# Performance work log

Measured on AMD Instinct MI355X. Metric: run time of the kernel, lower is better.

## Reference

```python
import jax, jax.numpy as jnp
import numpy as np

N = 20000   # nodes
D = 64      # emb_dim
H = 512     # 8 * emb_dim
E = 320000  # edges per graph


def setup_inputs() -> dict:
    key = jax.random.key(0)
    ks = jax.random.split(key, 40)
    i = iter(range(40))
    def nrm(shape, s=0.05):
        return jax.random.normal(ks[next(i)], shape, dtype=jnp.float32) * s
    def edges():
        return jax.random.randint(ks[next(i)], (E,), 0, N, dtype=jnp.int32)
    inp = {}
    inp['k_emb'] = nrm((N, D), 1.0)
    inp['pr_src'] = edges(); inp['pr_dst'] = edges()
    inp['pr_ew'] = jax.random.uniform(ks[next(i)], (E,), dtype=jnp.float32)
    inp['cc_src'] = edges(); inp['cc_dst'] = edges()
    inp['cc_ew'] = jax.random.uniform(ks[next(i)], (E,), dtype=jnp.float32)
    inp['sps_src'] = edges(); inp['sps_dst'] = edges()
    inp['pr_Ws0'] = nrm((D, H)); inp['pr_Wn0'] = nrm((D, H)); inp['pr_b0'] = jnp.zeros((H,), jnp.float32)
    inp['pr_Ws1'] = nrm((H, D)); inp['pr_Wn1'] = nrm((H, D)); inp['pr_b1'] = jnp.zeros((D,), jnp.float32)
    inp['cc_Ws0'] = nrm((D, H)); inp['cc_Wn0'] = nrm((D, H)); inp['cc_b0'] = jnp.zeros((H,), jnp.float32)
    inp['cc_Ws1'] = nrm((H, D)); inp['cc_Wn1'] = nrm((H, D)); inp['cc_b1'] = jnp.zeros((D,), jnp.float32)
    inp['ap_Ws0'] = nrm((D, D)); inp['ap_Wn0'] = nrm((D, D)); inp['ap_b0'] = jnp.zeros((D,), jnp.float32)
    inp['ap_Ws1'] = nrm((D, D)); inp['ap_Wn1'] = nrm((D, D)); inp['ap_b1'] = jnp.zeros((D,), jnp.float32)
    inp['att_W'] = nrm((D, D)); inp['att_b'] = jnp.zeros((D,), jnp.float32)
    return inp


def _sage(x, src, dst, ew, Ws, Wn, b):
    # DGL SAGEConv 'mean': neigh = sum(w_e * h_src) / in_degree; out = x@Ws + neigh@Wn + b
    msg = x[src]                                  # [E, din] gather
    if ew is not None:
        msg = msg * ew[:, None]
    agg = jax.ops.segment_sum(msg, dst, num_segments=N)            # [N, din]
    deg = jax.ops.segment_sum(jnp.ones((msg.shape[0],), x.dtype), dst, num_segments=N)
    agg = agg / jnp.maximum(deg, 1.0)[:, None]
    return x @ Ws + agg @ Wn + b


def reference(k_emb, pr_src, pr_dst, pr_ew, cc_src, cc_dst, cc_ew, sps_src, sps_dst,
              pr_Ws0, pr_Wn0, pr_b0, pr_Ws1, pr_Wn1, pr_b1,
              cc_Ws0, cc_Wn0, cc_b0, cc_Ws1, cc_Wn1, cc_b1,
              ap_Ws0, ap_Wn0, ap_b0, ap_Ws1, ap_Wn1, ap_b1,
              att_W, att_b):
    pr = jax.nn.relu(_sage(k_emb, pr_src, pr_dst, pr_ew, pr_Ws0, pr_Wn0, pr_b0))
    pr = _sage(pr, pr_src, pr_dst, pr_ew, pr_Ws1, pr_Wn1, pr_b1)            # [N, D]
    cc = jax.nn.relu(_sage(k_emb, cc_src, cc_dst, cc_ew, cc_Ws0, cc_Wn0, cc_b0))
    cc = _sage(cc, cc_src, cc_dst, cc_ew, cc_Ws1, cc_Wn1, cc_b1)            # [N, D]
    ap = jax.nn.relu(_sage(k_emb, sps_src, sps_dst, None, ap_Ws0, ap_Wn0, ap_b0))
    ap = _sage(ap, sps_src, sps_dst, None, ap_Ws1, ap_Wn1, ap_b1)           # [N, D]
    # APATT fusion
    z = jnp.stack((pr, cc), axis=1)                      # [N, 2, D]
    proj = jnp.tanh(z @ att_W + att_b)                   # [N, 2, D]
    w = jnp.sum(ap[:, None, :] * proj, axis=-1, keepdims=True).mean(0)  # [2, 1]
    beta = jax.nn.softmax(w, axis=0)                     # [2, 1]
    return (beta * z).sum(axis=1)                        # [N, D]
```

## Files before the change

kernel.cpp:

```cpp
#include <hip/hip_runtime.h>

#define NN 20000
#define NP 20032
#define DD 64
#define HH 512
#define EE 320000
#define ATT_BLOCKS 625
#define BLOCKS_E (EE / 256)
#define CB 157
#define EPB 4096
#define B1_BLOCKS ((EE + EPB - 1) / EPB)
#define ZERO_N (3 * NN + 3 * CB)
#define ZERO_BLOCKS ((ZERO_N + 255) / 256)

typedef __attribute__((ext_vector_type(8))) short short8;
typedef __attribute__((ext_vector_type(4))) float f32x4;

__device__ __forceinline__ ushort f2bf(float f) {
    union { float f; unsigned u; } v; v.f = f;
    unsigned r = v.u + 0x7FFF + ((v.u >> 16) & 1);
    return (ushort)(r >> 16);
}
__device__ __forceinline__ float bf2f(ushort h) {
    union { unsigned u; float f; } v; v.u = ((unsigned)h) << 16;
    return v.f;
}

__global__ __launch_bounds__(256) void hist3(const int* __restrict__ d0,
                                             const int* __restrict__ d1,
                                             const int* __restrict__ d2,
                                             int* __restrict__ cnt) {
    int g = blockIdx.x / BLOCKS_E;
    int e = (blockIdx.x % BLOCKS_E) * 256 + threadIdx.x;
    const int* d = (g == 0) ? d0 : (g == 1) ? d1 : d2;
    if (e < EE) atomicAdd(&cnt[g * NN + d[e]], 1);
}

__global__ __launch_bounds__(1024) void scan_kernel(const int* __restrict__ cnt,
                                                    int* __restrict__ rowptr,
                                                    float* __restrict__ invd) {
    __shared__ int part[1024];
    int g = blockIdx.x;
    const int* c = cnt + g * NN;
    int* rp = rowptr + g * (NN + 1);
    int tid = threadIdx.x;
    const int CH = (NN + 1023) / 1024;
    int i0 = tid * CH;
    int s = 0;
    for (int i = 0; i < CH; ++i) { int idx = i0 + i; if (idx < NN) s += c[idx]; }
    part[tid] = s;
    __syncthreads();
    for (int off = 1; off < 1024; off <<= 1) {
        int v = (tid >= off) ? part[tid - off] : 0;
        __syncthreads();
        part[tid] += v;
        __syncthreads();
    }
    int run = (tid > 0) ? part[tid - 1] : 0;
    for (int i = 0; i < CH; ++i) {
        int idx = i0 + i;
        if (idx < NN) {
            int cv = c[idx];
            rp[idx] = run; run += cv;
            invd[g * NN + idx] = 1.0f / fmaxf((float)cv, 1.0f);
        }
    }
    if (tid == 1023) rp[NN] = part[1023];
}

__global__ __launch_bounds__(256) void bucket_coarse(
    const int* __restrict__ s0, const int* __restrict__ d0, const float* __restrict__ w0,
    const int* __restrict__ s1, const int* __restrict__ d1, const float* __restrict__ w1,
    const int* __restrict__ s2, const int* __restrict__ d2,
    const int* __restrict__ rowptr,
    int* __restrict__ ccur,
    int2* __restrict__ ce,
    ushort* __restrict__ cd) {
    __shared__ int cnt_s[CB];
    __shared__ int off_s[CB];
    __shared__ int pos_s[CB];
    __shared__ int gbase[CB];
    __shared__ int lsrc[EPB];
    __shared__ int lew[EPB];
    __shared__ ushort ldst[EPB];
    int g = blockIdx.x / B1_BLOCKS;
    int blk = blockIdx.x % B1_BLOCKS;
    const int* S = (g == 0) ? s0 : (g == 1) ? s1 : s2;
    const int* D = (g == 0) ? d0 : (g == 1) ? d1 : d2;
    const float* W = (g == 0) ? w0 : (g == 1) ? w1 : nullptr;
    int e0 = blk * EPB;
    int n = min(EPB, EE - e0);
    for (int i = threadIdx.x; i < CB; i += 256) cnt_s[i] = 0;
    __syncthreads();
    for (int i = threadIdx.x; i < n; i += 256)
        atomicAdd(&cnt_s[D[e0 + i] >> 7], 1);
    __syncthreads();
    if (threadIdx.x == 0) {
        int run = 0;
        for (int i = 0; i < CB; ++i) { off_s[i] = run; run += cnt_s[i]; }
    }
    __syncthreads();
    if (threadIdx.x < CB) pos_s[threadIdx.x] = off_s[threadIdx.x];
    __syncthreads();
    for (int i = threadIdx.x; i < n; i += 256) {
        int e = e0 + i;
        int d = D[e];
        int p = atomicAdd(&pos_s[d >> 7], 1);
        lsrc[p] = S[e];
        lew[p] = (g < 2) ? __float_as_int(W[e]) : 0;
        ldst[p] = (ushort)d;
    }
    __syncthreads();
    if (threadIdx.x < CB)
        gbase[threadIdx.x] = atomicAdd(&ccur[g * CB + threadIdx.x], cnt_s[threadIdx.x]);
    __syncthreads();
    const int* rp = rowptr + g * (NN + 1);
    for (int j = threadIdx.x; j < n; j += 256) {
        ushort d = ldst[j];
        int cb = d >> 7;
        int gpos = rp[cb << 7] + gbase[cb] + (j - off_s[cb]);
        ce[(size_t)g * EE + gpos] = make_int2(lsrc[j], lew[j]);
        cd[(size_t)g * EE + gpos] = d;
    }
}

__global__ __launch_bounds__(256) void bucket_fine(
    const int* __restrict__ rowptr,
    const int2* __restrict__ ce, const ushort* __restrict__ cd,
    int2* __restrict__ edge_s,
    int* __restrict__ src_s2) {
    __shared__ int rp_s[129];
    __shared__ int cur_s[128];
    int g = blockIdx.x / CB;
    int cb = blockIdx.x % CB;
    const int* rp = rowptr + g * (NN + 1);
    int n0 = cb << 7;
    int n1 = min(n0 + 128, NN);
    int m = n1 - n0;
    if (threadIdx.x <= m) rp_s[threadIdx.x] = rp[n0 + threadIdx.x];
    if (threadIdx.x < m) cur_s[threadIdx.x] = 0;
    __syncthreads();
    int beg = rp_s[0], end = rp_s[m];
    for (int j = beg + threadIdx.x; j < end; j += 256) {
        int2 e = ce[(size_t)g * EE + j];
        int dl = (int)cd[(size_t)g * EE + j] - n0;
        int pos = rp_s[dl] + atomicAdd(&cur_s[dl], 1);
        if (g < 2) edge_s[(size_t)g * EE + pos] = e;
        else src_s2[pos] = e.x;
    }
}

__global__ __launch_bounds__(256) void pull_cast3(const ushort* __restrict__ xh,
                                                  const int* __restrict__ rowptr,
                                                  const int2* __restrict__ edge_s,
                                                  const int* __restrict__ src_s2,
                                                  const float* __restrict__ invd,
                                                  ushort* __restrict__ aggh) {
    int wid = (blockIdx.x * blockDim.x + threadIdx.x) >> 6;
    int lane = threadIdx.x & 63;
    if (wid >= 3 * NN) return;
    int g = wid / NN, n = wid % NN;
    const int* rp = rowptr + g * (NN + 1);
    int beg = rp[n], end = rp[n + 1];
    float a[8] = {};
    int i = beg;
    if (g < 2) {
        const int2* es = edge_s + (size_t)g * EE;
        for (; i + 8 <= end; i += 8) {
#pragma unroll
            for (int j = 0; j < 8; ++j) {
                int2 e = es[i + j];
                a[j] = fmaf(bf2f(xh[e.x * DD + lane]), __int_as_float(e.y), a[j]);
            }
        }
        for (; i < end; ++i) {
            int2 e = es[i];
            a[0] = fmaf(bf2f(xh[e.x * DD + lane]), __int_as_float(e.y), a[0]);
        }
    } else {
        for (; i + 8 <= end; i += 8) {
#pragma unroll
            for (int j = 0; j < 8; ++j)
                a[j] += bf2f(xh[src_s2[i + j] * DD + lane]);
        }
        for (; i < end; ++i) a[0] += bf2f(xh[src_s2[i] * DD + lane]);
    }
    float acc = ((a[0] + a[1]) + (a[2] + a[3])) + ((a[4] + a[5]) + (a[6] + a[7]));
    aggh[((size_t)g * NP + n) * 64 + lane] = f2bf(acc * invd[g * NN + n]);
}

__global__ __launch_bounds__(256) void pull_combine3(const ushort* __restrict__ xnh,
                                                     const int* __restrict__ rowptr,
                                                     const int2* __restrict__ edge_s,
                                                     const int* __restrict__ src_s2,
                                                     const float* __restrict__ invd,
                                                     const float* __restrict__ b_pr,
                                                     const float* __restrict__ b_cc,
                                                     const float* __restrict__ b_ap,
                                                     float* __restrict__ o_pr,
                                                     float* __restrict__ o_cc,
                                                     float* __restrict__ o_ap) {
    int wid = (blockIdx.x * blockDim.x + threadIdx.x) >> 6;
    int lane = threadIdx.x & 63;
    if (wid >= 3 * NN) return;
    int g = wid / NN, n = wid % NN;
    const int* rp = rowptr + g * (NN + 1);
    const ushort* x = xnh + (size_t)g * NP * 64;
    const float* bias = (g == 0) ? b_pr : (g == 1) ? b_cc : b_ap;
    float* out = (g == 0) ? o_pr : (g == 1) ? o_cc : o_ap;
    int beg = rp[n], end = rp[n + 1];
    float a[8] = {};
    int i = beg;
    if (g < 2) {
        const int2* es = edge_s + (size_t)g * EE;
        for (; i + 8 <= end; i += 8) {
#pragma unroll
            for (int j = 0; j < 8; ++j) {
                int2 e = es[i + j];
                a[j] = fmaf(bf2f(x[e.x * DD + lane]), __int_as_float(e.y), a[j]);
            }
        }
        for (; i < end; ++i) {
            int2 e = es[i];
            a[0] = fmaf(bf2f(x[e.x * DD + lane]), __int_as_float(e.y), a[0]);
        }
    } else {
        for (; i + 8 <= end; i += 8) {
#pragma unroll
            for (int j = 0; j < 8; ++j)
                a[j] += bf2f(x[src_s2[i + j] * DD + lane]);
        }
        for (; i < end; ++i) a[0] += bf2f(x[src_s2[i] * DD + lane]);
    }
    float acc = ((a[0] + a[1]) + (a[2] + a[3])) + ((a[4] + a[5]) + (a[6] + a[7]));
    out[n * DD + lane] += acc * invd[g * NN + n] + bias[lane];
}

__global__ __launch_bounds__(256) void pack_all(
    const float* __restrict__ pr_Ws0, const float* __restrict__ pr_Wn0,
    const float* __restrict__ cc_Ws0, const float* __restrict__ cc_Wn0,
    const float* __restrict__ pr_Ws1, const float* __restrict__ pr_Wn1,
    const float* __restrict__ cc_Ws1, const float* __restrict__ cc_Wn1,
    const float* __restrict__ ap_Ws0, const float* __restrict__ ap_Wn0,
    const float* __restrict__ ap_Ws1, const float* __restrict__ ap_Wn1,
    const float* __restrict__ k_emb,
    ushort* __restrict__ W0h_pr, ushort* __restrict__ W0h_cc,
    ushort* __restrict__ W1h_pr, ushort* __restrict__ W1h_cc,
    ushort* __restrict__ W0h_ap, ushort* __restrict__ W1h_ap,
    ushort* __restrict__ xh,
    int* __restrict__ zero_base) {
    int b = blockIdx.x;
    int tid = threadIdx.x;
    if (b < 512) {
        int t = (b & 255) * 256 + tid;
        const float* Ws = (b < 256) ? pr_Ws0 : cc_Ws0;
        const float* Wn = (b < 256) ? pr_Wn0 : cc_Wn0;
        ushort* o = (b < 256) ? W0h_pr : W0h_cc;
        int c = t >> 7, k = t & 127;
        o[t] = f2bf((k < 64) ? Ws[k * 512 + c] : Wn[(k - 64) * 512 + c]);
    } else if (b < 1024) {
        int t = ((b - 512) & 255) * 256 + tid;
        const float* Ws = (b < 768) ? pr_Ws1 : cc_Ws1;
        const float* Wn = (b < 768) ? pr_Wn1 : cc_Wn1;
        ushort* o = (b < 768) ? W1h_pr : W1h_cc;
        int c = t >> 9, k = t & 511;
        o[t] = f2bf((c < 64) ? Ws[k * 64 + c] : Wn[k * 64 + (c - 64)]);
    } else if (b < 1056) {
        int t = (b - 1024) * 256 + tid;
        int c = t >> 7, k = t & 127;
        W0h_ap[t] = f2bf((k < 64) ? ap_Ws0[k * 64 + c] : ap_Wn0[(k - 64) * 64 + c]);
    } else if (b < 1088) {
        int t = (b - 1056) * 256 + tid;
        int c = t >> 6, k = t & 63;
        W1h_ap[t] = f2bf((c < 64) ? ap_Ws1[k * 64 + c] : ap_Wn1[k * 64 + (c - 64)]);
    } else if (b < 1088 + ZERO_BLOCKS) {
        int t = (b - 1088) * 256 + tid;
        if (t < ZERO_N) zero_base[t] = 0;
    } else {
        int t = (b - 1088 - ZERO_BLOCKS) * 256 + tid;
        if (t < NN * DD) xh[t] = f2bf(k_emb[t]);
    }
}

__global__ __launch_bounds__(512, 4) void fused_sage4(
    const ushort* __restrict__ xh,
    const ushort* __restrict__ aggA,
    const ushort* __restrict__ W0a, const ushort* __restrict__ W1a,
    const ushort* __restrict__ W0b, const ushort* __restrict__ W1b,
    const float* __restrict__ b0a, const float* __restrict__ b0b,
    float* __restrict__ outS0, float* __restrict__ outS1,
    ushort* __restrict__ xnh, int nblk) {
    constexpr int LROW = 136;
    __shared__ ushort Ahs[64 * LROW];
    __shared__ ushort h1s[64 * LROW];
    int br = blockIdx.x / nblk;
    int rb = blockIdx.x % nblk;
    const ushort* W0 = br ? W0b : W0a;
    const ushort* W1 = br ? W1b : W1a;
    const float* b0 = br ? b0b : b0a;
    float* outS = br ? outS1 : outS0;
    ushort* outX = xnh + (size_t)br * NP * 64;
    const ushort* agg = aggA + (size_t)br * NP * 64;
    int row0 = rb * 64;

    int wv = threadIdx.x >> 6;
    int lane = threadIdx.x & 63;
    int lrow = lane & 15;
    int koff = (lane >> 4) * 8;
    int crow = (lane >> 4) * 4;

    {
        int r = threadIdx.x >> 3;
        int seg = threadIdx.x & 7;
        const ushort* src = (seg < 4) ? (xh + (size_t)(row0 + r) * 64 + seg * 16)
                                      : (agg + (size_t)(row0 + r) * 64 + (seg - 4) * 16);
        *(short8*)&Ahs[r * LROW + seg * 16] = *(const short8*)src;
        *(short8*)&Ahs[r * LROW + seg * 16 + 8] = *(const short8*)(src + 8);
    }
    __syncthreads();

    f32x4 C[4] = {};
#pragma unroll
    for (int p = 0; p < 4; ++p) {
        {
            short8 B[4];
#pragma unroll
            for (int kk = 0; kk < 4; ++kk)
                B[kk] = *(const short8*)(W0 + (size_t)(p * 128 + wv * 16 + lrow) * 128 + kk * 32 + koff);
            f32x4 acc[4] = {};
#pragma unroll
            for (int rg = 0; rg < 4; ++rg) {
#pragma unroll
                for (int kk = 0; kk < 4; ++kk) {
                    short8 a = *(const short8*)&Ahs[(rg * 16 + lrow) * LROW + kk * 32 + koff];
                    acc[rg] = __builtin_amdgcn_mfma_f32_16x16x32_bf16(a, B[kk], acc[rg], 0, 0, 0);
                }
            }
            float bb = b0[p * 128 + wv * 16 + lrow];
#pragma unroll
            for (int rg = 0; rg < 4; ++rg) {
#pragma unroll
                for (int r = 0; r < 4; ++r) {
                    float v = fmaxf(acc[rg][r] + bb, 0.0f);
                    h1s[(rg * 16 + crow + r) * LROW + wv * 16 + lrow] = f2bf(v);
                }
            }
        }
        __syncthreads();
        {
            short8 B[4];
#pragma unroll
            for (int kc = 0; kc < 4; ++kc)
                B[kc] = *(const short8*)(W1 + (size_t)(wv * 16 + lrow) * HH + p * 128 + kc * 32 + koff);
#pragma unroll
            for (int rg = 0; rg < 4; ++rg) {
#pragma unroll
                for (int kc = 0; kc < 4; ++kc) {
                    short8 a = *(const short8*)&h1s[(rg * 16 + lrow) * LROW + kc * 32 + koff];
                    C[rg] = __builtin_amdgcn_mfma_f32_16x16x32_bf16(a, B[kc], C[rg], 0, 0, 0);
                }
            }
        }
        __syncthreads();
    }
    int col = wv * 16 + lrow;
    if (col < 64) {
        float* o = outS + col;
#pragma unroll
        for (int rg = 0; rg < 4; ++rg)
#pragma unroll
            for (int r = 0; r < 4; ++r) {
                int row = row0 + rg * 16 + crow + r;
                if (row < NN) o[(size_t)row * 64] = C[rg][r];
            }
    } else {
        ushort* o = outX + (col - 64);
#pragma unroll
        for (int rg = 0; rg < 4; ++rg)
#pragma unroll
            for (int r = 0; r < 4; ++r) {
                int row = row0 + rg * 16 + crow + r;
                if (row < NN) o[(size_t)row * 64] = f2bf(C[rg][r]);
            }
    }
}

__global__ __launch_bounds__(256, 4) void fused_sage_ap(
    const ushort* __restrict__ xh,
    const ushort* __restrict__ agg,
    const ushort* __restrict__ W0,
    const ushort* __restrict__ W1,
    const float* __restrict__ b0,
    float* __restrict__ outS,
    ushort* __restrict__ outX) {
    constexpr int LROW = 72;
    __shared__ ushort h1s[16 * LROW];
    int wv = threadIdx.x >> 6;
    int lane = threadIdx.x & 63;
    int lrow = lane & 15;
    int koff = (lane >> 4) * 8;
    int crow = (lane >> 4) * 4;
    int row0 = blockIdx.x * 16;

    {
        const size_t aoff = (size_t)(row0 + lrow) * 64 + koff;
        short8 aF[4];
#pragma unroll
        for (int kk = 0; kk < 2; ++kk) {
            aF[kk]     = *(const short8*)(xh + aoff + kk * 32);
            aF[2 + kk] = *(const short8*)(agg + aoff + kk * 32);
        }
        f32x4 acc = {};
#pragma unroll
        for (int kk = 0; kk < 4; ++kk) {
            short8 b = *(const short8*)(W0 + (size_t)(wv * 16 + lrow) * 128 + kk * 32 + koff);
            acc = __builtin_amdgcn_mfma_f32_16x16x32_bf16(aF[kk], b, acc, 0, 0, 0);
        }
        float bb = b0[wv * 16 + lrow];
#pragma unroll
        for (int r = 0; r < 4; ++r) {
            h1s[(crow + r) * LROW + wv * 16 + lrow] = f2bf(fmaxf(acc[r] + bb, 0.0f));
        }
    }
    __syncthreads();
    {
        f32x4 C2[2] = {};
#pragma unroll
        for (int kc = 0; kc < 2; ++kc) {
            short8 a = *(const short8*)&h1s[lrow * LROW + kc * 32 + koff];
#pragma unroll
            for (int c = 0; c < 2; ++c) {
                short8 b = *(const short8*)(W1 + (size_t)(wv * 32 + c * 16 + lrow) * 64 + kc * 32 + koff);
                C2[c] = __builtin_amdgcn_mfma_f32_16x16x32_bf16(a, b, C2[c], 0, 0, 0);
            }
        }
#pragma unroll
        for (int c = 0; c < 2; ++c) {
            int col = wv * 32 + c * 16 + lrow;
#pragma unroll
            for (int r = 0; r < 4; ++r) {
                int row = row0 + crow + r;
                if (row < NN) {
                    if (col < 64) outS[(size_t)row * 64 + col] = C2[c][r];
                    else outX[(size_t)row * 64 + (col - 64)] = f2bf(C2[c][r]);
                }
            }
        }
    }
}

__global__ __launch_bounds__(256) void att_stage1(const float* __restrict__ pr,
                                                  const float* __restrict__ cc,
                                                  const float* __restrict__ ap,
                                                  const float* __restrict__ attW,
                                                  const float* __restrict__ attb,
                                                  float2* __restrict__ partial) {
    __shared__ float red[8];
    int lane = threadIdx.x & 63;
    int wv = threadIdx.x >> 6;
    int gw = blockIdx.x * 4 + wv;
    const int nwaves = ATT_BLOCKS * 4;
    float b = attb[lane];
    float c0 = 0.f, c1 = 0.f;
    for (int n = gw; n < NN; n += nwaves) {
        float p0 = 0.f, p1 = 0.f;
        for (int k = 0; k < DD; ++k) {
            float w = attW[k * DD + lane];
            p0 = fmaf(pr[n * DD + k], w, p0);
            p1 = fmaf(cc[n * DD + k], w, p1);
        }
        float a = ap[n * DD + lane];
        c0 += a * tanhf(p0 + b);
        c1 += a * tanhf(p1 + b);
    }
#pragma unroll
    for (int off = 32; off; off >>= 1) {
        c0 += __shfl_xor(c0, off);
        c1 += __shfl_xor(c1, off);
    }
    if (lane == 0) { red[wv * 2] = c0; red[wv * 2 + 1] = c1; }
    __syncthreads();
    if (threadIdx.x == 0) {
        partial[blockIdx.x] = make_float2(red[0] + red[2] + red[4] + red[6],
                                          red[1] + red[3] + red[5] + red[7]);
    }
}

__global__ __launch_bounds__(64) void att_stage2(const float2* __restrict__ partial,
                                                 float* __restrict__ w_acc) {
    int lane = threadIdx.x;
    float s0 = 0.f, s1 = 0.f;
    for (int i = lane; i < ATT_BLOCKS; i += 64) {
        float2 p = partial[i];
        s0 += p.x; s1 += p.y;
    }
#pragma unroll
    for (int off = 32; off; off >>= 1) {
        s0 += __shfl_xor(s0, off);
        s1 += __shfl_xor(s1, off);
    }
    if (lane == 0) { w_acc[0] = s0; w_acc[1] = s1; }
}

__global__ __launch_bounds__(256) void final_kernel(float* __restrict__ pr_out,
                                                    const float* __restrict__ cc,
                                                    const float* __restrict__ w_acc) {
    int t = blockIdx.x * blockDim.x + threadIdx.x;
    if (t >= NN * DD) return;
    float w0 = w_acc[0] * (1.0f / NN);
    float w1 = w_acc[1] * (1.0f / NN);
    float m = fmaxf(w0, w1);
    float e0 = __expf(w0 - m), e1 = __expf(w1 - m);
    float inv = 1.0f / (e0 + e1);
    pr_out[t] = (e0 * pr_out[t] + e1 * cc[t]) * inv;
}

extern "C" void kernel_launch(void* const* d_in, const int* in_sizes, int n_in,
                              void* d_out, int out_size, void* d_ws, size_t ws_size,
                              hipStream_t stream) {
    const float* k_emb  = (const float*)d_in[0];
    const int*   pr_src = (const int*)d_in[1];
    const int*   pr_dst = (const int*)d_in[2];
    const float* pr_ew  = (const float*)d_in[3];
    const int*   cc_src = (const int*)d_in[4];
    const int*   cc_dst = (const int*)d_in[5];
    const float* cc_ew  = (const float*)d_in[6];
    const int*   sps_src = (const int*)d_in[7];
    const int*   sps_dst = (const int*)d_in[8];
    const float* pr_Ws0 = (const float*)d_in[9];
    const float* pr_Wn0 = (const float*)d_in[10];
    const float* pr_b0  = (const float*)d_in[11];
    const float* pr_Ws1 = (const float*)d_in[12];
    const float* pr_Wn1 = (const float*)d_in[13];
    const float* pr_b1  = (const float*)d_in[14];
    const float* cc_Ws0 = (const float*)d_in[15];
    const float* cc_Wn0 = (const float*)d_in[16];
    const float* cc_b0  = (const float*)d_in[17];
    const float* cc_Ws1 = (const float*)d_in[18];
    const float* cc_Wn1 = (const float*)d_in[19];
    const float* cc_b1  = (const float*)d_in[20];
    const float* ap_Ws0 = (const float*)d_in[21];
    const float* ap_Wn0 = (const float*)d_in[22];
    const float* ap_b0  = (const float*)d_in[23];
    const float* ap_Ws1 = (const float*)d_in[24];
    const float* ap_Wn1 = (const float*)d_in[25];
    const float* ap_b1  = (const float*)d_in[26];
    const float* att_W  = (const float*)d_in[27];
    const float* att_b  = (const float*)d_in[28];
    float* out = (float*)d_out;

    char* base = (char*)d_ws;
    size_t off = 0;
    auto alloc = [&](size_t bytes) -> void* {
        void* p = base + off;
        off = (off + bytes + 255) & ~(size_t)255;
        return p;
    };
    float*  invd   = (float*)alloc((size_t)3 * NN * 4);
    int*    cnt    = (int*)alloc((size_t)ZERO_N * 4);
    int*    ccur   = cnt + 3 * NN;
    int*    rowptr = (int*)alloc((size_t)3 * (NN + 1) * 4);
    int2*   edge_s = (int2*)alloc((size_t)2 * EE * 8);
    int*    src_s2 = (int*)alloc((size_t)EE * 4);
    int2*   ce     = (int2*)alloc((size_t)3 * EE * 8);
    ushort* cd     = (ushort*)alloc((size_t)3 * EE * 2);
    float*  w_acc  = (float*)alloc(64);
    float2* att_partial = (float2*)alloc(ATT_BLOCKS * 8);
    ushort* xnh    = (ushort*)alloc((size_t)3 * NP * DD * 2);
    float*  out_cc = (float*)alloc((size_t)NN * DD * 4);
    float*  out_ap = (float*)alloc((size_t)NN * DD * 4);
    ushort* xh     = (ushort*)alloc((size_t)NP * DD * 2);
    ushort* aggh   = (ushort*)alloc((size_t)3 * NP * DD * 2);
    ushort* W0h_pr = (ushort*)alloc(512 * 128 * 2);
    ushort* W0h_cc = (ushort*)alloc(512 * 128 * 2);
    ushort* W0h_ap = (ushort*)alloc(64 * 128 * 2);
    ushort* W1h_pr = (ushort*)alloc(128 * 512 * 2);
    ushort* W1h_cc = (ushort*)alloc(128 * 512 * 2);
    ushort* W1h_ap = (ushort*)alloc(128 * 64 * 2);
    float*  out_pr = out;

    const int TB = 256;
    const int blocks_ND = (NN * DD) / TB;
    const int blocks_pull3 = (3 * NN * 64) / TB;
    const int NBLK64 = NP / 64;

    pack_all<<<1088 + ZERO_BLOCKS + blocks_ND, TB, 0, stream>>>(
        pr_Ws0, pr_Wn0, cc_Ws0, cc_Wn0, pr_Ws1, pr_Wn1, cc_Ws1, cc_Wn1,
        ap_Ws0, ap_Wn0, ap_Ws1, ap_Wn1, k_emb,
        W0h_pr, W0h_cc, W1h_pr, W1h_cc, W0h_ap, W1h_ap, xh, cnt);

    hist3<<<3 * BLOCKS_E, TB, 0, stream>>>(pr_dst, cc_dst, sps_dst, cnt);
    scan_kernel<<<3, 1024, 0, stream>>>(cnt, rowptr, invd);
    bucket_coarse<<<3 * B1_BLOCKS, TB, 0, stream>>>(pr_src, pr_dst, pr_ew,
                                                    cc_src, cc_dst, cc_ew,
                                                    sps_src, sps_dst,
                                                    rowptr, ccur, ce, cd);
    bucket_fine<<<3 * CB, TB, 0, stream>>>(rowptr, ce, cd, edge_s, src_s2);

    pull_cast3<<<blocks_pull3, TB, 0, stream>>>(xh, rowptr, edge_s, src_s2, invd, aggh);

    fused_sage4<<<2 * NBLK64, 512, 0, stream>>>(
        xh, aggh,
        W0h_pr, W1h_pr, W0h_cc, W1h_cc,
        pr_b0, cc_b0, out_pr, out_cc, xnh, NBLK64);
    fused_sage_ap<<<NP / 16, 256, 0, stream>>>(
        xh, aggh + (size_t)2 * NP * 64,
        W0h_ap, W1h_ap, ap_b0, out_ap, xnh + (size_t)2 * NP * 64);

    pull_combine3<<<blocks_pull3, TB, 0, stream>>>(xnh, rowptr, edge_s, src_s2, invd,
                                                   pr_b1, cc_b1, ap_b1,
                                                   out_pr, out_cc, out_ap);

    att_stage1<<<ATT_BLOCKS, TB, 0, stream>>>(out_pr, out_cc, out_ap, att_W, att_b, att_partial);
    att_stage2<<<1, 64, 0, stream>>>(att_partial, w_acc);
    final_kernel<<<blocks_ND, TB, 0, stream>>>(out_pr, out_cc, w_acc);
}
```

Baseline: 285.8 us.

## Pack edges into 32-bit words with fp16 weights and split pulls across two waves

Edge records shrink from int2 (src, fp32 weight) to one 32-bit word holding a 16-bit source index and an fp16 weight. The unweighted graph's source list also drops to ushort. This cuts bytes moved in the bucketing and pull kernels. Each node's neighbour list is now split between two waves that combine their partial sums through shared memory, which doubles the parallelism of the gather. The risks are reduced edge-weight precision and a hard dependence on N fitting in 16 bits, plus an added block-wide sync.

Result: slower. 300.4 us (+5.1%).

```diff
diff --git a/kernel.cpp b/kernel.cpp
--- a/kernel.cpp
+++ b/kernel.cpp
@@ -1,4 +1,5 @@
 #include <hip/hip_runtime.h>
+#include <hip/hip_fp16.h>
 
 #define NN 20000
 #define NP 20032
@@ -24,6 +25,10 @@
 __device__ __forceinline__ float bf2f(ushort h) {
     union { unsigned u; float f; } v; v.u = ((unsigned)h) << 16;
     return v.f;
+}
+__device__ __forceinline__ float ew_of(uint w) {
+    __half h = __ushort_as_half((ushort)(w >> 16));
+    return __half2float(h);
 }
 
 __global__ __launch_bounds__(256) void hist3(const int* __restrict__ d0,
@@ -74,14 +79,13 @@
     const int* __restrict__ s2, const int* __restrict__ d2,
     const int* __restrict__ rowptr,
     int* __restrict__ ccur,
-    int2* __restrict__ ce,
+    uint* __restrict__ ce,
     ushort* __restrict__ cd) {
     __shared__ int cnt_s[CB];
     __shared__ int off_s[CB];
     __shared__ int pos_s[CB];
     __shared__ int gbase[CB];
-    __shared__ int lsrc[EPB];
-    __shared__ int lew[EPB];
+    __shared__ uint lword[EPB];
     __shared__ ushort ldst[EPB];
     int g = blockIdx.x / B1_BLOCKS;
     int blk = blockIdx.x % B1_BLOCKS;
@@ -106,8 +110,8 @@
         int e = e0 + i;
         int d = D[e];
         int p = atomicAdd(&pos_s[d >> 7], 1);
-        lsrc[p] = S[e];
-        lew[p] = (g < 2) ? __float_as_int(W[e]) : 0;
+        ushort ewh = (g < 2) ? __half_as_ushort(__float2half(W[e])) : 0;
+        lword[p] = ((uint)ewh << 16) | (uint)(S[e] & 0xFFFF);
         ldst[p] = (ushort)d;
     }
     __syncthreads();
@@ -119,16 +123,16 @@
         ushort d = ldst[j];
         int cb = d >> 7;
         int gpos = rp[cb << 7] + gbase[cb] + (j - off_s[cb]);
-        ce[(size_t)g * EE + gpos] = make_int2(lsrc[j], lew[j]);
+        ce[(size_t)g * EE + gpos] = lword[j];
         cd[(size_t)g * EE + gpos] = d;
     }
 }
 
 __global__ __launch_bounds__(256) void bucket_fine(
     const int* __restrict__ rowptr,
-    const int2* __restrict__ ce, const ushort* __restrict__ cd,
-    int2* __restrict__ edge_s,
-    int* __restrict__ src_s2) {
+    const uint* __restrict__ ce, const ushort* __restrict__ cd,
+    uint* __restrict__ edge_s,
+    ushort* __restrict__ src_s2) {
     __shared__ int rp_s[129];
     __shared__ int cur_s[128];
     int g = blockIdx.x / CB;
@@ -142,57 +146,70 @@
     __syncthreads();
     int beg = rp_s[0], end = rp_s[m];
     for (int j = beg + threadIdx.x; j < end; j += 256) {
-        int2 e = ce[(size_t)g * EE + j];
+        uint e = ce[(size_t)g * EE + j];
         int dl = (int)cd[(size_t)g * EE + j] - n0;
         int pos = rp_s[dl] + atomicAdd(&cur_s[dl], 1);
         if (g < 2) edge_s[(size_t)g * EE + pos] = e;
-        else src_s2[pos] = e.x;
+        else src_s2[pos] = (ushort)(e & 0xFFFF);
     }
 }
 
 __global__ __launch_bounds__(256) void pull_cast3(const ushort* __restrict__ xh,
                                                   const int* __restrict__ rowptr,
-                                                  const int2* __restrict__ edge_s,
-                                                  const int* __restrict__ src_s2,
+                                                  const uint* __restrict__ edge_s,
+                                                  const ushort* __restrict__ src_s2,
                                                   const float* __restrict__ invd,
                                                   ushort* __restrict__ aggh) {
-    int wid = (blockIdx.x * blockDim.x + threadIdx.x) >> 6;
+    __shared__ float part[2][64];
+    int gwave = (blockIdx.x * 256 + threadIdx.x) >> 6;
     int lane = threadIdx.x & 63;
-    if (wid >= 3 * NN) return;
-    int g = wid / NN, n = wid % NN;
+    int wv = threadIdx.x >> 6;
+    int pairIdx = wv >> 1;
+    int sub = wv & 1;
+    int node = gwave >> 1;
+    if (node >= 3 * NN) return;
+    int g = node / NN, n = node % NN;
     const int* rp = rowptr + g * (NN + 1);
     int beg = rp[n], end = rp[n + 1];
-    float a[8] = {};
-    int i = beg;
+    int mid = (beg + end + 1) >> 1;
+    int lo = sub ? mid : beg;
+    int hi = sub ? end : mid;
+    float a[4] = {};
+    int i = lo;
     if (g < 2) {
-        const int2* es = edge_s + (size_t)g * EE;
-        for (; i + 8 <= end; i += 8) {
-#pragma unroll
-            for (int j = 0; j < 8; ++j) {
-                int2 e = es[i + j];
-                a[j] = fmaf(bf2f(xh[e.x * DD + lane]), __int_as_float(e.y), a[j]);
-            }
-        }
-        for (; i < end; ++i) {
-            int2 e = es[i];
-            a[0] = fmaf(bf2f(xh[e.x * DD + lane]), __int_as_float(e.y), a[0]);
+        const uint* es = edge_s + (size_t)g * EE;
+        for (; i + 4 <= hi; i += 4) {
+#pragma unroll
+            for (int j = 0; j < 4; ++j) {
+                uint e = es[i + j];
+                a[j] = fmaf(bf2f(xh[(e & 0xFFFF) * DD + lane]), ew_of(e), a[j]);
+            }
+        }
+        for (; i < hi; ++i) {
+            uint e = es[i];
+            a[0] = fmaf(bf2f(xh[(e & 0xFFFF) * DD + lane]), ew_of(e), a[0]);
         }
     } else {
-        for (; i + 8 <= end; i += 8) {
-#pragma unroll
-            for (int j = 0; j < 8; ++j)
-                a[j] += bf2f(xh[src_s2[i + j] * DD + lane]);
-        }
-        for (; i < end; ++i) a[0] += bf2f(xh[src_s2[i] * DD + lane]);
-    }
-    float acc = ((a[0] + a[1]) + (a[2] + a[3])) + ((a[4] + a[5]) + (a[6] + a[7]));
-    aggh[((size_t)g * NP + n) * 64 + lane] = f2bf(acc * invd[g * NN + n]);
+        for (; i + 4 <= hi; i += 4) {
+#pragma unroll
+            for (int j = 0; j < 4; ++j)
+                a[j] += bf2f(xh[(int)src_s2[i + j] * DD + lane]);
+        }
+        for (; i < hi; ++i) a[0] += bf2f(xh[(int)src_s2[i] * DD + lane]);
+    }
+    float acc = (a[0] + a[1]) + (a[2] + a[3]);
+    if (sub == 1) part[pairIdx][lane] = acc;
+    __syncthreads();
+    if (sub == 0) {
+        acc += part[pairIdx][lane];
+        aggh[((size_t)g * NP + n) * 64 + lane] = f2bf(acc * invd[g * NN + n]);
+    }
 }
 
 __global__ __launch_bounds__(256) void pull_combine3(const ushort* __restrict__ xnh,
                                                      const int* __restrict__ rowptr,
-                                                     const int2* __restrict__ edge_s,
-                                                     const int* __restrict__ src_s2,
+                                                     const uint* __restrict__ edge_s,
+                                                     const ushort* __restrict__ src_s2,
                                                      const float* __restrict__ invd,
                                                      const float* __restrict__ b_pr,
                                                      const float* __restrict__ b_cc,
@@ -200,40 +217,53 @@
                                                      float* __restrict__ o_pr,
                                                      float* __restrict__ o_cc,
                                                      float* __restrict__ o_ap) {
-    int wid = (blockIdx.x * blockDim.x + threadIdx.x) >> 6;
+    __shared__ float part[2][64];
+    int gwave = (blockIdx.x * 256 + threadIdx.x) >> 6;
     int lane = threadIdx.x & 63;
-    if (wid >= 3 * NN) return;
-    int g = wid / NN, n = wid % NN;
+    int wv = threadIdx.x >> 6;
+    int pairIdx = wv >> 1;
+    int sub = wv & 1;
+    int node = gwave >> 1;
+    if (node >= 3 * NN) return;
+    int g = node / NN, n = node % NN;
     const int* rp = rowptr + g * (NN + 1);
     const ushort* x = xnh + (size_t)g * NP * 64;
-    const float* bias = (g == 0) ? b_pr : (g == 1) ? b_cc : b_ap;
-    float* out = (g == 0) ? o_pr : (g == 1) ? o_cc : o_ap;
     int beg = rp[n], end = rp[n + 1];
-    float a[8] = {};
-    int i = beg;
+    int mid = (beg + end + 1) >> 1;
+    int lo = sub ? mid : beg;
+    int hi = sub ? end : mid;
+    float a[4] = {};
+    int i = lo;
     if (g < 2) {
-        const int2* es = edge_s + (size_t)g * EE;
-        for (; i + 8 <= end; i += 8) {
-#pragma unroll
-            for (int j = 0; j < 8; ++j) {
-                int2 e = es[i + j];
-                a[j] = fmaf(bf2f(x[e.x * DD + lane]), __int_as_float(e.y), a[j]);
-            }
-        }
-        for (; i < end; ++i) {
-            int2 e = es[i];
-            a[0] = fmaf(bf2f(x[e.x * DD + lane]), __int_as_float(e.y), a[0]);
+        const uint* es = edge_s + (size_t)g * EE;
+        for (; i + 4 <= hi; i += 4) {
+#pragma unroll
+            for (int j = 0; j < 4; ++j) {
+                uint e = es[i + j];
+                a[j] = fmaf(bf2f(x[(e & 0xFFFF) * DD + lane]), ew_of(e), a[j]);
+            }
+        }
+        for (; i < hi; ++i) {
+            uint e = es[i];
+            a[0] = fmaf(bf2f(x[(e & 0xFFFF) * DD + lane]), ew_of(e), a[0]);
         }
     } else {
-        for (; i + 8 <= end; i += 8) {
-#pragma unroll
-            for (int j = 0; j < 8; ++j)
-                a[j] += bf2f(x[src_s2[i + j] * DD + lane]);
-        }
-        for (; i < end; ++i) a[0] += bf2f(x[src_s2[i] * DD + lane]);
-    }
-    float acc = ((a[0] + a[1]) + (a[2] + a[3])) + ((a[4] + a[5]) + (a[6] + a[7]));
-    out[n * DD + lane] += acc * invd[g * NN + n] + bias[lane];
+        for (; i + 4 <= hi; i += 4) {
+#pragma unroll
+            for (int j = 0; j < 4; ++j)
+                a[j] += bf2f(x[(int)src_s2[i + j] * DD + lane]);
+        }
+        for (; i < hi; ++i) a[0] += bf2f(x[(int)src_s2[i] * DD + lane]);
+    }
+    float acc = (a[0] + a[1]) + (a[2] + a[3]);
+    if (sub == 1) part[pairIdx][lane] = acc;
+    __syncthreads();
+    if (sub == 0) {
+        acc += part[pairIdx][lane];
+        const float* bias = (g == 0) ? b_pr : (g == 1) ? b_cc : b_ap;
+        float* out = (g == 0) ? o_pr : (g == 1) ? o_cc : o_ap;
+        out[n * DD + lane] += acc * invd[g * NN + n] + bias[lane];
+    }
 }
 
 __global__ __launch_bounds__(256) void pack_all(
@@ -560,9 +590,9 @@
     int*    cnt    = (int*)alloc((size_t)ZERO_N * 4);
     int*    ccur   = cnt + 3 * NN;
     int*    rowptr = (int*)alloc((size_t)3 * (NN + 1) * 4);
-    int2*   edge_s = (int2*)alloc((size_t)2 * EE * 8);
-    int*    src_s2 = (int*)alloc((size_t)EE * 4);
-    int2*   ce     = (int2*)alloc((size_t)3 * EE * 8);
+    uint*   edge_s = (uint*)alloc((size_t)2 * EE * 4);
+    ushort* src_s2 = (ushort*)alloc((size_t)EE * 2);
+    uint*   ce     = (uint*)alloc((size_t)3 * EE * 4);
     ushort* cd     = (ushort*)alloc((size_t)3 * EE * 2);
     float*  w_acc  = (float*)alloc(64);
     float2* att_partial = (float2*)alloc(ATT_BLOCKS * 8);
@@ -581,7 +611,7 @@
 
     const int TB = 256;
     const int blocks_ND = (NN * DD) / TB;
-    const int blocks_pull3 = (3 * NN * 64) / TB;
+    const int blocks_pull = (3 * NN * 2 * 64) / TB;
     const int NBLK64 = NP / 64;
 
     pack_all<<<1088 + ZERO_BLOCKS + blocks_ND, TB, 0, stream>>>(
@@ -597,7 +627,7 @@
                                                     rowptr, ccur, ce, cd);
     bucket_fine<<<3 * CB, TB, 0, stream>>>(rowptr, ce, cd, edge_s, src_s2);
 
-    pull_cast3<<<blocks_pull3, TB, 0, stream>>>(xh, rowptr, edge_s, src_s2, invd, aggh);
+    pull_cast3<<<blocks_pull, TB, 0, stream>>>(xh, rowptr, edge_s, src_s2, invd, aggh);
 
     fused_sage4<<<2 * NBLK64, 512, 0, stream>>>(
         xh, aggh,
@@ -607,9 +637,9 @@
         xh, aggh + (size_t)2 * NP * 64,
         W0h_ap, W1h_ap, ap_b0, out_ap, xnh + (size_t)2 * NP * 64);
 
-    pull_combine3<<<blocks_pull3, TB, 0, stream>>>(xnh, rowptr, edge_s, src_s2, invd,
-                                                   pr_b1, cc_b1, ap_b1,
-                                                   out_pr, out_cc, out_ap);
+    pull_combine3<<<blocks_pull, TB, 0, stream>>>(xnh, rowptr, edge_s, src_s2, invd,
+                                                  pr_b1, cc_b1, ap_b1,
+                                                  out_pr, out_cc, out_ap);
 
     att_stage1<<<ATT_BLOCKS, TB, 0, stream>>>(out_pr, out_cc, out_ap, att_W, att_b, att_partial);
     att_stage2<<<1, 64, 0, stream>>>(att_partial, w_acc);
```
